# Kernel optimization log

Hardware: AMD Instinct MI355X
Metric: run time of the kernel (lower is better)

Reference implementation:

```python
import jax, jax.numpy as jnp
import numpy as np

N = 8192   # collocation points
H = 64     # hidden_dim (d_out of each KANLayer)
UH = 8     # unary_hidden_dim


def setup_inputs() -> dict:
    key = jax.random.key(0)
    ks = jax.random.split(key, 16)
    d = {}
    d["x"] = jax.random.normal(ks[0], (N, 1), dtype=jnp.float32)
    d["t"] = jax.random.normal(ks[1], (N, 1), dtype=jnp.float32)
    dims = [(2, H), (H, H), (H, H)]  # (d_in, d_out) per KANLayer
    idx = 2
    for l, (di, do) in enumerate(dims):
        d[f"W1_{l}"] = jax.random.normal(ks[idx], (do, di, UH), dtype=jnp.float32) * 0.5; idx += 1
        d[f"B1_{l}"] = jax.random.normal(ks[idx], (do, di, UH), dtype=jnp.float32) * 0.1; idx += 1
        d[f"W2_{l}"] = jax.random.normal(ks[idx], (do, di, UH), dtype=jnp.float32) * 0.5; idx += 1
        d[f"B2_{l}"] = jax.random.normal(ks[idx], (do, di), dtype=jnp.float32) * 0.1; idx += 1
    d["W_out"] = jax.random.normal(ks[14], (1, H), dtype=jnp.float32) * 0.1
    d["b_out"] = jnp.zeros((1,), dtype=jnp.float32)
    return d


def kan_layer(h, W1, B1, W2, B2):
    """Stacked KANLayer: y[n,j] = sum_i ( W2[j,i,:] . tanh(h[n,i]*W1[j,i,:] + B1[j,i,:]) + B2[j,i] ).
    h: (N, d_in); W1,B1,W2: (d_out, d_in, UH); B2: (d_out, d_in). Returns (N, d_out)."""
    hid = jnp.tanh(h[:, None, :, None] * W1[None] + B1[None])  # (N, d_out, d_in, UH)
    return jnp.einsum('ndih,dih->nd', hid, W2) + B2.sum(axis=1)


def reference(x, t, W1_0, B1_0, W2_0, B2_0, W1_1, B1_1, W2_1, B2_1,
              W1_2, B1_2, W2_2, B2_2, W_out, b_out):
    h = jnp.concatenate([x, t], axis=1)  # (N, 2)
    layers = [(W1_0, B1_0, W2_0, B2_0),
              (W1_1, B1_1, W2_1, B2_1),
              (W1_2, B1_2, W2_2, B2_2)]
    for W1, B1, W2, B2 in layers:
        h = jnp.tanh(kan_layer(h, W1, B1, W2, B2))
    u = h @ W_out.T + b_out  # (N, 1)
    return u
```

## Files before the change

kernel.cpp:

```cpp
#include <hip/hip_runtime.h>
#include <math.h>


#define C2L 2.88539008177792681472f
#define P_CHEB 16
#define M_SAMP 32

__device__ __forceinline__ float tanh_hw(float z) {
  float e = __builtin_amdgcn_exp2f(z * C2L);
  float r = __builtin_amdgcn_rcpf(1.0f + e);
  return fmaf(r, -2.0f, 1.0f);
}

__global__ __launch_bounds__(256) void kan_prep(
    const float* __restrict__ W1_1, const float* __restrict__ B1_1,
    const float* __restrict__ W2_1, const float* __restrict__ B2_1,
    const float* __restrict__ W1_2, const float* __restrict__ B1_2,
    const float* __restrict__ W2_2, const float* __restrict__ B2_2,
    float* __restrict__ G1, float* __restrict__ G2)
{
  const int g = blockIdx.x * 256 + threadIdx.x;
  const int k = g & 7;
  const int ji = (g >> 3) & 4095;
  const int layer = g >> 15;
  const float* __restrict__ W1 = layer ? W1_2 : W1_1;
  const float* __restrict__ B1 = layer ? B1_2 : B1_1;
  const float* __restrict__ W2 = layer ? W2_2 : W2_1;
  const float* __restrict__ B2 = layer ? B2_2 : B2_1;
  float* __restrict__ G = layer ? G2 : G1;

  const float w  = W1[ji * 8 + k];
  const float b  = B1[ji * 8 + k];
  const float w2 = W2[ji * 8 + k];

  float acc[P_CHEB];
#pragma unroll
  for (int p = 0; p < P_CHEB; ++p) acc[p] = 0.f;

  for (int m = 0; m < M_SAMP; ++m) {
    const float theta = ((float)m + 0.5f) * (3.14159265358979323846f / M_SAMP);
    const float c = cosf(theta);
    const float s = w2 * tanh_hw(fmaf(w, c, b));
    acc[0] += s;
    acc[1] = fmaf(s, c, acc[1]);
    const float c2 = c + c;
    float tp0 = 1.f, tp1 = c;
#pragma unroll
    for (int p = 2; p < P_CHEB; ++p) {
      const float t = fmaf(c2, tp1, -tp0);
      acc[p] = fmaf(s, t, acc[p]);
      tp0 = tp1; tp1 = t;
    }
  }
#pragma unroll
  for (int p = 0; p < P_CHEB; ++p) {
    float v = acc[p] * ((p == 0) ? (1.f / M_SAMP) : (2.f / M_SAMP));
    v += __shfl_xor(v, 1);
    v += __shfl_xor(v, 2);
    v += __shfl_xor(v, 4);
    acc[p] = v;
  }
  if (k == 0) {
    float* __restrict__ dst = G + ji * P_CHEB;
    acc[0] += B2[ji];
#pragma unroll
    for (int p = 0; p < P_CHEB; ++p) dst[p] = acc[p];
  }
}

__global__ __launch_bounds__(256) void kan_layer0(
    const float* __restrict__ x, const float* __restrict__ t,
    const float* __restrict__ W1, const float* __restrict__ B1,
    const float* __restrict__ W2, const float* __restrict__ B2,
    const float* __restrict__ bout,
    float* __restrict__ hA,
    float* __restrict__ out)
{
  const int tid  = threadIdx.x;
  const int lane = tid & 63;
  const int wave = __builtin_amdgcn_readfirstlane(tid >> 6);
  const int bx = blockIdx.x, by = blockIdx.y;
  const int flat = by * 128 + bx;
  if (flat < 32) out[flat * 256 + tid] = bout[0];

  const int n = bx * 64 + lane;
  const int j = by * 4 + wave;
  const float hx = x[n], ht = t[n];
  float a0 = B2[j * 2 + 0];
  float a1 = B2[j * 2 + 1];
#pragma unroll
  for (int k = 0; k < 8; ++k) {
    float z0 = fmaf(hx, W1[j * 16 + k], B1[j * 16 + k]);
    a0 = fmaf(W2[j * 16 + k], tanh_hw(z0), a0);
    float z1 = fmaf(ht, W1[j * 16 + 8 + k], B1[j * 16 + 8 + k]);
    a1 = fmaf(W2[j * 16 + 8 + k], tanh_hw(z1), a1);
  }
  hA[j * 8192 + n] = tanh_hw(a0 + a1);
}

template <int HEAD>
__global__ __launch_bounds__(512, 6) void kan_cheb(
    const float* __restrict__ hin,
    const float* __restrict__ G,
    const float* __restrict__ Wout,
    float* __restrict__ outp)
{
  __shared__ float  hs[64][64];
  __shared__ float4 Gs[8 * 256];
  __shared__ float  redA[8][64];
  __shared__ float  redB[8][64];
  const int tid  = threadIdx.x;
  const int lane = tid & 63;
  const int wave = __builtin_amdgcn_readfirstlane(tid >> 6);
  const int n    = blockIdx.x * 64 + lane;

#pragma unroll
  for (int r = 0; r < 8; ++r) {
    const int i = r * 8 + wave;
    hs[i][lane] = hin[i * 8192 + n];
  }
  {
    const float4* __restrict__ gsrc = (const float4*)(G + blockIdx.y * 8 * 64 * P_CHEB);
#pragma unroll
    for (int q = 0; q < 4; ++q) Gs[q * 512 + tid] = gsrc[q * 512 + tid];
  }
  __syncthreads();

  const int jloc = (wave & 3) * 2;
  const int jA = blockIdx.y * 8 + jloc;
  const int jB = jA + 1;
  const int ihalf = wave >> 2;
  const float4* __restrict__ gaq = &Gs[jloc * 256];
  const float4* __restrict__ gbq = &Gs[(jloc + 1) * 256];

  float aA0 = 0.f, aA1 = 0.f, aB0 = 0.f, aB1 = 0.f;
  const int i0 = ihalf * 32;
  for (int i = i0; i < i0 + 32; ++i) {
    const float h  = hs[i][lane];
    const float h2 = h + h;
    const float t2  = fmaf(h2, h,  -1.f);
    const float d2  = t2 + t2;
    const float t3  = fmaf(h2, t2, -h);
    const float t4  = fmaf(d2, t2, -1.f);
    const float d3  = t3 + t3;
    const float d4  = t4 + t4;
    const float t5  = fmaf(d3, t2, -h);
    const float t6  = fmaf(d3, t3, -1.f);
    const float t7  = fmaf(d4, t3, -h);
    const float t8  = fmaf(d4, t4, -1.f);
    const float d5  = t5 + t5;
    const float d6  = t6 + t6;
    const float d7  = t7 + t7;
    const float d8  = t8 + t8;
    const float t9  = fmaf(d5, t4, -h);
    const float t10 = fmaf(d5, t5, -1.f);
    const float t11 = fmaf(d6, t5, -h);
    const float t12 = fmaf(d6, t6, -1.f);
    const float t13 = fmaf(d7, t6, -h);
    const float t14 = fmaf(d7, t7, -1.f);
    const float t15 = fmaf(d8, t7, -h);

    const float4 va0 = gaq[i * 4 + 0];
    const float4 va1 = gaq[i * 4 + 1];
    const float4 va2 = gaq[i * 4 + 2];
    const float4 va3 = gaq[i * 4 + 3];
    aA0 += va0.x;
    aA1 = fmaf(va0.y, h,   aA1);
    aA0 = fmaf(va0.z, t2,  aA0);
    aA1 = fmaf(va0.w, t3,  aA1);
    aA0 = fmaf(va1.x, t4,  aA0);
    aA1 = fmaf(va1.y, t5,  aA1);
    aA0 = fmaf(va1.z, t6,  aA0);
    aA1 = fmaf(va1.w, t7,  aA1);
    aA0 = fmaf(va2.x, t8,  aA0);
    aA1 = fmaf(va2.y, t9,  aA1);
    aA0 = fmaf(va2.z, t10, aA0);
    aA1 = fmaf(va2.w, t11, aA1);
    aA0 = fmaf(va3.x, t12, aA0);
    aA1 = fmaf(va3.y, t13, aA1);
    aA0 = fmaf(va3.z, t14, aA0);
    aA1 = fmaf(va3.w, t15, aA1);

    const float4 vb0 = gbq[i * 4 + 0];
    const float4 vb1 = gbq[i * 4 + 1];
    const float4 vb2 = gbq[i * 4 + 2];
    const float4 vb3 = gbq[i * 4 + 3];
    aB0 += vb0.x;
    aB1 = fmaf(vb0.y, h,   aB1);
    aB0 = fmaf(vb0.z, t2,  aB0);
    aB1 = fmaf(vb0.w, t3,  aB1);
    aB0 = fmaf(vb1.x, t4,  aB0);
    aB1 = fmaf(vb1.y, t5,  aB1);
    aB0 = fmaf(vb1.z, t6,  aB0);
    aB1 = fmaf(vb1.w, t7,  aB1);
    aB0 = fmaf(vb2.x, t8,  aB0);
    aB1 = fmaf(vb2.y, t9,  aB1);
    aB0 = fmaf(vb2.z, t10, aB0);
    aB1 = fmaf(vb2.w, t11, aB1);
    aB0 = fmaf(vb3.x, t12, aB0);
    aB1 = fmaf(vb3.y, t13, aB1);
    aB0 = fmaf(vb3.z, t14, aB0);
    aB1 = fmaf(vb3.w, t15, aB1);
  }

  redA[wave][lane] = aA0 + aA1;
  redB[wave][lane] = aB0 + aB1;
  __syncthreads();

  if (HEAD) {
    if (wave < 4) {
      const float yA = redA[wave][lane] + redA[wave + 4][lane];
      const float yB = redB[wave][lane] + redB[wave + 4][lane];
      redA[wave][lane] = tanh_hw(yA) * Wout[jA] + tanh_hw(yB) * Wout[jB];
    }
    __syncthreads();
    if (wave == 0) {
      atomicAdd(&outp[n], (redA[0][lane] + redA[1][lane]) +
                          (redA[2][lane] + redA[3][lane]));
    }
  } else {
    if (wave < 4) {
      const float yA = redA[wave][lane] + redA[wave + 4][lane];
      const float yB = redB[wave][lane] + redB[wave + 4][lane];
      outp[jA * 8192 + n] = tanh_hw(yA);
      outp[jB * 8192 + n] = tanh_hw(yB);
    }
  }
}

extern "C" void kernel_launch(void* const* d_in, const int* in_sizes, int n_in,
                              void* d_out, int out_size, void* d_ws, size_t ws_size,
                              hipStream_t stream) {
  const float* x    = (const float*)d_in[0];
  const float* t    = (const float*)d_in[1];
  const float* W1_0 = (const float*)d_in[2];
  const float* B1_0 = (const float*)d_in[3];
  const float* W2_0 = (const float*)d_in[4];
  const float* B2_0 = (const float*)d_in[5];
  const float* W1_1 = (const float*)d_in[6];
  const float* B1_1 = (const float*)d_in[7];
  const float* W2_1 = (const float*)d_in[8];
  const float* B2_1 = (const float*)d_in[9];
  const float* W1_2 = (const float*)d_in[10];
  const float* B1_2 = (const float*)d_in[11];
  const float* W2_2 = (const float*)d_in[12];
  const float* B2_2 = (const float*)d_in[13];
  const float* Wout = (const float*)d_in[14];
  const float* bout = (const float*)d_in[15];
  float* out = (float*)d_out;

  float* hA = (float*)d_ws;
  float* hB = hA + 64 * 8192;
  float* G1 = hB + 64 * 8192;
  float* G2 = G1 + 64 * 64 * P_CHEB;

  kan_prep<<<dim3(256), 256, 0, stream>>>(
      W1_1, B1_1, W2_1, B2_1, W1_2, B1_2, W2_2, B2_2, G1, G2);
  kan_layer0<<<dim3(128, 16), 256, 0, stream>>>(
      x, t, W1_0, B1_0, W2_0, B2_0, bout, hA, out);
  kan_cheb<0><<<dim3(128, 8), 512, 0, stream>>>(hA, G1, Wout, hB);
  kan_cheb<1><<<dim3(128, 8), 512, 0, stream>>>(hB, G2, Wout, out);
}
```

Before: 141.0 us.

## Process four point groups per block to reuse Chebyshev coefficient loads

The Chebyshev layer kernel now handles 256 points per block (four groups of 64) instead of 64. Each coefficient vector loaded from shared memory is reused across the four groups, cutting LDS traffic per FMA, and the grid shrinks from 128x8 to 32x8 blocks. In exchange, shared memory per block grows to about 112 KB and occupancy falls, leaving only 256 blocks, which may underfill the GPU's compute units.

```diff
diff --git a/kernel.cpp b/kernel.cpp
--- a/kernel.cpp
+++ b/kernel.cpp
@@ -99,30 +99,31 @@
 }
 
 template <int HEAD>
-__global__ __launch_bounds__(512, 6) void kan_cheb(
+__global__ __launch_bounds__(512, 2) void kan_cheb4(
     const float* __restrict__ hin,
     const float* __restrict__ G,
     const float* __restrict__ Wout,
     float* __restrict__ outp)
 {
-  __shared__ float  hs[64][64];
-  __shared__ float4 Gs[8 * 256];
-  __shared__ float  redA[8][64];
-  __shared__ float  redB[8][64];
+  __shared__ float hsb[4 * 64 * 64];
+  __shared__ float Gsb[8 * 64 * 16];
+  __shared__ float redA[8][64][4];
+  __shared__ float redB[8][64][4];
   const int tid  = threadIdx.x;
   const int lane = tid & 63;
   const int wave = __builtin_amdgcn_readfirstlane(tid >> 6);
-  const int n    = blockIdx.x * 64 + lane;
-
-#pragma unroll
-  for (int r = 0; r < 8; ++r) {
-    const int i = r * 8 + wave;
-    hs[i][lane] = hin[i * 8192 + n];
+  const int n0   = blockIdx.x * 256;
+
+  for (int rr = 0; rr < 32; ++rr) {
+    const int row = rr * 8 + wave;
+    const int q = row >> 6, i = row & 63;
+    hsb[row * 64 + lane] = hin[i * 8192 + n0 + q * 64 + lane];
   }
   {
     const float4* __restrict__ gsrc = (const float4*)(G + blockIdx.y * 8 * 64 * P_CHEB);
-#pragma unroll
-    for (int q = 0; q < 4; ++q) Gs[q * 512 + tid] = gsrc[q * 512 + tid];
+    float4* __restrict__ gdst = (float4*)Gsb;
+#pragma unroll
+    for (int qq = 0; qq < 4; ++qq) gdst[qq * 512 + tid] = gsrc[qq * 512 + tid];
   }
   __syncthreads();
 
@@ -130,100 +131,121 @@
   const int jA = blockIdx.y * 8 + jloc;
   const int jB = jA + 1;
   const int ihalf = wave >> 2;
-  const float4* __restrict__ gaq = &Gs[jloc * 256];
-  const float4* __restrict__ gbq = &Gs[(jloc + 1) * 256];
-
-  float aA0 = 0.f, aA1 = 0.f, aB0 = 0.f, aB1 = 0.f;
+  const float4* __restrict__ gA = (const float4*)(Gsb + jloc * 64 * 16);
+  const float4* __restrict__ gB = (const float4*)(Gsb + (jloc + 1) * 64 * 16);
+
+  float accA[4] = {0.f, 0.f, 0.f, 0.f};
+  float accB[4] = {0.f, 0.f, 0.f, 0.f};
+
   const int i0 = ihalf * 32;
   for (int i = i0; i < i0 + 32; ++i) {
-    const float h  = hs[i][lane];
-    const float h2 = h + h;
-    const float t2  = fmaf(h2, h,  -1.f);
-    const float d2  = t2 + t2;
-    const float t3  = fmaf(h2, t2, -h);
-    const float t4  = fmaf(d2, t2, -1.f);
-    const float d3  = t3 + t3;
-    const float d4  = t4 + t4;
-    const float t5  = fmaf(d3, t2, -h);
-    const float t6  = fmaf(d3, t3, -1.f);
-    const float t7  = fmaf(d4, t3, -h);
-    const float t8  = fmaf(d4, t4, -1.f);
-    const float d5  = t5 + t5;
-    const float d6  = t6 + t6;
-    const float d7  = t7 + t7;
-    const float d8  = t8 + t8;
-    const float t9  = fmaf(d5, t4, -h);
-    const float t10 = fmaf(d5, t5, -1.f);
-    const float t11 = fmaf(d6, t5, -h);
-    const float t12 = fmaf(d6, t6, -1.f);
-    const float t13 = fmaf(d7, t6, -h);
-    const float t14 = fmaf(d7, t7, -1.f);
-    const float t15 = fmaf(d8, t7, -h);
-
-    const float4 va0 = gaq[i * 4 + 0];
-    const float4 va1 = gaq[i * 4 + 1];
-    const float4 va2 = gaq[i * 4 + 2];
-    const float4 va3 = gaq[i * 4 + 3];
-    aA0 += va0.x;
-    aA1 = fmaf(va0.y, h,   aA1);
-    aA0 = fmaf(va0.z, t2,  aA0);
-    aA1 = fmaf(va0.w, t3,  aA1);
-    aA0 = fmaf(va1.x, t4,  aA0);
-    aA1 = fmaf(va1.y, t5,  aA1);
-    aA0 = fmaf(va1.z, t6,  aA0);
-    aA1 = fmaf(va1.w, t7,  aA1);
-    aA0 = fmaf(va2.x, t8,  aA0);
-    aA1 = fmaf(va2.y, t9,  aA1);
-    aA0 = fmaf(va2.z, t10, aA0);
-    aA1 = fmaf(va2.w, t11, aA1);
-    aA0 = fmaf(va3.x, t12, aA0);
-    aA1 = fmaf(va3.y, t13, aA1);
-    aA0 = fmaf(va3.z, t14, aA0);
-    aA1 = fmaf(va3.w, t15, aA1);
-
-    const float4 vb0 = gbq[i * 4 + 0];
-    const float4 vb1 = gbq[i * 4 + 1];
-    const float4 vb2 = gbq[i * 4 + 2];
-    const float4 vb3 = gbq[i * 4 + 3];
-    aB0 += vb0.x;
-    aB1 = fmaf(vb0.y, h,   aB1);
-    aB0 = fmaf(vb0.z, t2,  aB0);
-    aB1 = fmaf(vb0.w, t3,  aB1);
-    aB0 = fmaf(vb1.x, t4,  aB0);
-    aB1 = fmaf(vb1.y, t5,  aB1);
-    aB0 = fmaf(vb1.z, t6,  aB0);
-    aB1 = fmaf(vb1.w, t7,  aB1);
-    aB0 = fmaf(vb2.x, t8,  aB0);
-    aB1 = fmaf(vb2.y, t9,  aB1);
-    aB0 = fmaf(vb2.z, t10, aB0);
-    aB1 = fmaf(vb2.w, t11, aB1);
-    aB0 = fmaf(vb3.x, t12, aB0);
-    aB1 = fmaf(vb3.y, t13, aB1);
-    aB0 = fmaf(vb3.z, t14, aB0);
-    aB1 = fmaf(vb3.w, t15, aB1);
-  }
-
-  redA[wave][lane] = aA0 + aA1;
-  redB[wave][lane] = aB0 + aB1;
+    const float4 va0 = gA[i * 4 + 0];
+    const float4 va1 = gA[i * 4 + 1];
+    const float4 va2 = gA[i * 4 + 2];
+    const float4 va3 = gA[i * 4 + 3];
+    const float4 vb0 = gB[i * 4 + 0];
+    const float4 vb1 = gB[i * 4 + 1];
+    const float4 vb2 = gB[i * 4 + 2];
+    const float4 vb3 = gB[i * 4 + 3];
+#pragma unroll
+    for (int q = 0; q < 4; ++q) {
+      const float h  = hsb[(q * 64 + i) * 64 + lane];
+      const float h2 = h + h;
+      const float t2  = fmaf(h2, h,  -1.f);
+      const float d2  = t2 + t2;
+      const float t3  = fmaf(h2, t2, -h);
+      const float t4  = fmaf(d2, t2, -1.f);
+      const float d3  = t3 + t3;
+      const float d4  = t4 + t4;
+      const float t5  = fmaf(d3, t2, -h);
+      const float t6  = fmaf(d3, t3, -1.f);
+      const float t7  = fmaf(d4, t3, -h);
+      const float t8  = fmaf(d4, t4, -1.f);
+      const float d5  = t5 + t5;
+      const float d6  = t6 + t6;
+      const float d7  = t7 + t7;
+      const float d8  = t8 + t8;
+      const float t9  = fmaf(d5, t4, -h);
+      const float t10 = fmaf(d5, t5, -1.f);
+      const float t11 = fmaf(d6, t5, -h);
+      const float t12 = fmaf(d6, t6, -1.f);
+      const float t13 = fmaf(d7, t6, -h);
+      const float t14 = fmaf(d7, t7, -1.f);
+      const float t15 = fmaf(d8, t7, -h);
+
+      float sA = va0.x;
+      sA = fmaf(va0.y, h,   sA);
+      sA = fmaf(va0.z, t2,  sA);
+      sA = fmaf(va0.w, t3,  sA);
+      sA = fmaf(va1.x, t4,  sA);
+      sA = fmaf(va1.y, t5,  sA);
+      sA = fmaf(va1.z, t6,  sA);
+      sA = fmaf(va1.w, t7,  sA);
+      sA = fmaf(va2.x, t8,  sA);
+      sA = fmaf(va2.y, t9,  sA);
+      sA = fmaf(va2.z, t10, sA);
+      sA = fmaf(va2.w, t11, sA);
+      sA = fmaf(va3.x, t12, sA);
+      sA = fmaf(va3.y, t13, sA);
+      sA = fmaf(va3.z, t14, sA);
+      sA = fmaf(va3.w, t15, sA);
+      accA[q] += sA;
+
+      float sB = vb0.x;
+      sB = fmaf(vb0.y, h,   sB);
+      sB = fmaf(vb0.z, t2,  sB);
+      sB = fmaf(vb0.w, t3,  sB);
+      sB = fmaf(vb1.x, t4,  sB);
+      sB = fmaf(vb1.y, t5,  sB);
+      sB = fmaf(vb1.z, t6,  sB);
+      sB = fmaf(vb1.w, t7,  sB);
+      sB = fmaf(vb2.x, t8,  sB);
+      sB = fmaf(vb2.y, t9,  sB);
+      sB = fmaf(vb2.z, t10, sB);
+      sB = fmaf(vb2.w, t11, sB);
+      sB = fmaf(vb3.x, t12, sB);
+      sB = fmaf(vb3.y, t13, sB);
+      sB = fmaf(vb3.z, t14, sB);
+      sB = fmaf(vb3.w, t15, sB);
+      accB[q] += sB;
+    }
+  }
+
+#pragma unroll
+  for (int q = 0; q < 4; ++q) {
+    redA[wave][lane][q] = accA[q];
+    redB[wave][lane][q] = accB[q];
+  }
   __syncthreads();
 
   if (HEAD) {
     if (wave < 4) {
-      const float yA = redA[wave][lane] + redA[wave + 4][lane];
-      const float yB = redB[wave][lane] + redB[wave + 4][lane];
-      redA[wave][lane] = tanh_hw(yA) * Wout[jA] + tanh_hw(yB) * Wout[jB];
+      const float wA = Wout[jA], wB = Wout[jB];
+#pragma unroll
+      for (int q = 0; q < 4; ++q) {
+        const float yA = redA[wave][lane][q] + redA[wave + 4][lane][q];
+        const float yB = redB[wave][lane][q] + redB[wave + 4][lane][q];
+        redA[wave][lane][q] = tanh_hw(yA) * wA + tanh_hw(yB) * wB;
+      }
     }
     __syncthreads();
     if (wave == 0) {
-      atomicAdd(&outp[n], (redA[0][lane] + redA[1][lane]) +
-                          (redA[2][lane] + redA[3][lane]));
+#pragma unroll
+      for (int q = 0; q < 4; ++q) {
+        const float s = (redA[0][lane][q] + redA[1][lane][q]) +
+                        (redA[2][lane][q] + redA[3][lane][q]);
+        atomicAdd(&outp[n0 + q * 64 + lane], s);
+      }
     }
   } else {
     if (wave < 4) {
-      const float yA = redA[wave][lane] + redA[wave + 4][lane];
-      const float yB = redB[wave][lane] + redB[wave + 4][lane];
-      outp[jA * 8192 + n] = tanh_hw(yA);
-      outp[jB * 8192 + n] = tanh_hw(yB);
+#pragma unroll
+      for (int q = 0; q < 4; ++q) {
+        const float yA = redA[wave][lane][q] + redA[wave + 4][lane][q];
+        const float yB = redB[wave][lane][q] + redB[wave + 4][lane][q];
+        outp[jA * 8192 + n0 + q * 64 + lane] = tanh_hw(yA);
+        outp[jB * 8192 + n0 + q * 64 + lane] = tanh_hw(yB);
+      }
     }
   }
 }
@@ -258,6 +280,6 @@
       W1_1, B1_1, W2_1, B2_1, W1_2, B1_2, W2_2, B2_2, G1, G2);
   kan_layer0<<<dim3(128, 16), 256, 0, stream>>>(
       x, t, W1_0, B1_0, W2_0, B2_0, bout, hA, out);
-  kan_cheb<0><<<dim3(128, 8), 512, 0, stream>>>(hA, G1, Wout, hB);
-  kan_cheb<1><<<dim3(128, 8), 512, 0, stream>>>(hB, G2, Wout, out);
-}
+  kan_cheb4<0><<<dim3(32, 8), 512, 0, stream>>>(hA, G1, Wout, hB);
+  kan_cheb4<1><<<dim3(32, 8), 512, 0, stream>>>(hB, G2, Wout, out);
+}
```

Result: faster. 134.2 us (-4.8%).
